# Optimization experiments

Hardware: AMD Instinct MI355X
Metric: run time of the kernel (lower is better)

## Reference

```python
import jax, jax.numpy as jnp
import numpy as np

BANK = 64
SHAPE = (512, 2048)
BATCH = 64
SELECTED = 4


def setup_inputs() -> dict:
    key = jax.random.key(0)
    k1, k2, k3 = jax.random.split(key, 3)
    parameter = jax.random.normal(k1, (*SHAPE, BANK), dtype=jnp.float32)
    selection_index = jax.random.randint(k2, (BATCH, SELECTED), 0, BANK)
    selection_probabilities = jax.random.uniform(k3, (BATCH, SELECTED), dtype=jnp.float32)
    return {
        "parameter": parameter,
        "selection_index": selection_index,
        "selection_probabilities": selection_probabilities,
    }


def reference(parameter, selection_index, selection_probabilities):
    # parameter: (*SHAPE, bank) -> move bank dim to front: (bank, *SHAPE)
    banked = jnp.moveaxis(parameter, -1, 0)
    # gather selected banks: (batch, selected, *SHAPE)
    gathered = banked[selection_index]
    # weighted sum over the selected dim (probabilities broadcast over data dims)
    out = jnp.einsum("bsij,bs->bij", gathered, selection_probabilities)
    return out
```

## Files before the change

kernel.cpp:

```cpp
#include <hip/hip_runtime.h>


#define NPOS   (512 * 2048)
#define NBANK  64
#define NBATCH 64
#define TILE   256
#define BLK    512

typedef float  f32x4 __attribute__((ext_vector_type(4)));
typedef int    i32x4 __attribute__((ext_vector_type(4)));

__global__ __launch_bounds__(BLK, 4) void vparam_kernel(
    const float* __restrict__ param,
    const int*   __restrict__ sel,
    const float* __restrict__ prob,
    float*       __restrict__ out)
{
    __shared__ float lds[NBANK * TILE];

    const int tid       = threadIdx.x;
    const int tile_base = blockIdx.x * TILE;

    const f32x4* g4 = (const f32x4*)(param + (size_t)tile_base * NBANK);
    #pragma unroll
    for (int i = 0; i < 8; ++i) {
        f32x4 v = __builtin_nontemporal_load(&g4[i * BLK + tid]);
        int p  = i * 32 + (tid >> 4);
        int k0 = (tid & 15) * 4;
        #pragma unroll
        for (int j = 0; j < 4; ++j) {
            int k = k0 + j;
            lds[k * TILE + (p ^ (k & 28))] = v[j];
        }
    }
    __syncthreads();

    const int wave = tid >> 6;
    const int lane = tid & 63;
    const int pw   = lane * 4;
    const i32x4* sel4  = (const i32x4*)sel;
    const f32x4* prob4 = (const f32x4*)prob;

    #pragma unroll
    for (int j = 0; j < 8; ++j) {
        int b = __builtin_amdgcn_readfirstlane(wave * 8 + j);
        i32x4 iv = sel4[b];
        f32x4 wv = prob4[b];
        const f32x4 a0 = *(const f32x4*)&lds[iv.x * TILE + (pw ^ (iv.x & 28))];
        const f32x4 a1 = *(const f32x4*)&lds[iv.y * TILE + (pw ^ (iv.y & 28))];
        const f32x4 a2 = *(const f32x4*)&lds[iv.z * TILE + (pw ^ (iv.z & 28))];
        const f32x4 a3 = *(const f32x4*)&lds[iv.w * TILE + (pw ^ (iv.w & 28))];
        f32x4 acc = a0 * wv.x + a1 * wv.y + a2 * wv.z + a3 * wv.w;
        f32x4* o = (f32x4*)(out + (size_t)b * NPOS + tile_base);
        __builtin_nontemporal_store(acc, &o[lane]);
    }
}

extern "C" void kernel_launch(void* const* d_in, const int* in_sizes, int n_in,
                              void* d_out, int out_size, void* d_ws, size_t ws_size,
                              hipStream_t stream) {
    const float* param = (const float*)d_in[0];
    const int*   sel   = (const int*)d_in[1];
    const float* prob  = (const float*)d_in[2];
    float*       out   = (float*)d_out;

    dim3 grid(NPOS / TILE);
    vparam_kernel<<<grid, BLK, 0, stream>>>(param, sel, prob, out);
}
```

Baseline: 96.25 us.

## Persistent blocks with register-prefetched next tile overlapping compute and stores

Switches from one block per tile to a fixed grid of 512 persistent blocks, each processing 8 tiles in sequence. The next tile's parameter data is loaded into registers while the current tile is computed from LDS and written out, then committed to LDS after a barrier. This is meant to hide global load latency behind the output stores. It costs extra registers, and occupancy is lowered from 4 to 2 blocks per CU in the launch bounds.

```diff
diff --git a/kernel.cpp b/kernel.cpp
--- a/kernel.cpp
+++ b/kernel.cpp
@@ -6,11 +6,13 @@
 #define NBATCH 64
 #define TILE   256
 #define BLK    512
+#define NBLK   512
+#define TPB    (NPOS / TILE / NBLK)
 
-typedef float  f32x4 __attribute__((ext_vector_type(4)));
-typedef int    i32x4 __attribute__((ext_vector_type(4)));
+typedef float f32x4 __attribute__((ext_vector_type(4)));
+typedef int   i32x4 __attribute__((ext_vector_type(4)));
 
-__global__ __launch_bounds__(BLK, 4) void vparam_kernel(
+__global__ __launch_bounds__(BLK, 2) void vparam_kernel(
     const float* __restrict__ param,
     const int*   __restrict__ sel,
     const float* __restrict__ prob,
@@ -18,41 +20,74 @@
 {
     __shared__ float lds[NBANK * TILE];
 
-    const int tid       = threadIdx.x;
-    const int tile_base = blockIdx.x * TILE;
-
-    const f32x4* g4 = (const f32x4*)(param + (size_t)tile_base * NBANK);
-    #pragma unroll
-    for (int i = 0; i < 8; ++i) {
-        f32x4 v = __builtin_nontemporal_load(&g4[i * BLK + tid]);
-        int p  = i * 32 + (tid >> 4);
-        int k0 = (tid & 15) * 4;
-        #pragma unroll
-        for (int j = 0; j < 4; ++j) {
-            int k = k0 + j;
-            lds[k * TILE + (p ^ (k & 28))] = v[j];
-        }
-    }
-    __syncthreads();
-
+    const int tid  = threadIdx.x;
     const int wave = tid >> 6;
     const int lane = tid & 63;
     const int pw   = lane * 4;
+    const int sp   = tid >> 4;
+    const int k0   = (tid & 15) * 4;
+
     const i32x4* sel4  = (const i32x4*)sel;
     const f32x4* prob4 = (const f32x4*)prob;
 
-    #pragma unroll
-    for (int j = 0; j < 8; ++j) {
-        int b = __builtin_amdgcn_readfirstlane(wave * 8 + j);
-        i32x4 iv = sel4[b];
-        f32x4 wv = prob4[b];
-        const f32x4 a0 = *(const f32x4*)&lds[iv.x * TILE + (pw ^ (iv.x & 28))];
-        const f32x4 a1 = *(const f32x4*)&lds[iv.y * TILE + (pw ^ (iv.y & 28))];
-        const f32x4 a2 = *(const f32x4*)&lds[iv.z * TILE + (pw ^ (iv.z & 28))];
-        const f32x4 a3 = *(const f32x4*)&lds[iv.w * TILE + (pw ^ (iv.w & 28))];
-        f32x4 acc = a0 * wv.x + a1 * wv.y + a2 * wv.z + a3 * wv.w;
-        f32x4* o = (f32x4*)(out + (size_t)b * NPOS + tile_base);
-        __builtin_nontemporal_store(acc, &o[lane]);
+    f32x4 r[8];
+    int tile = blockIdx.x * TPB;
+
+    {
+        const f32x4* g4 = (const f32x4*)(param + (size_t)tile * (TILE * NBANK));
+        #pragma unroll
+        for (int i = 0; i < 8; ++i)
+            r[i] = __builtin_nontemporal_load(&g4[i * BLK + tid]);
+        #pragma unroll
+        for (int i = 0; i < 8; ++i) {
+            int p = i * 32 + sp;
+            #pragma unroll
+            for (int j = 0; j < 4; ++j) {
+                int k = k0 + j;
+                lds[k * TILE + (p ^ (k & 28))] = r[i][j];
+            }
+        }
+    }
+
+    #pragma unroll 1
+    for (int t = 0; t < TPB; ++t) {
+        __syncthreads();
+
+        if (t + 1 < TPB) {
+            const f32x4* g4 = (const f32x4*)(param + (size_t)(tile + 1) * (TILE * NBANK));
+            #pragma unroll
+            for (int i = 0; i < 8; ++i)
+                r[i] = __builtin_nontemporal_load(&g4[i * BLK + tid]);
+        }
+
+        const size_t obase = (size_t)tile * TILE;
+        #pragma unroll
+        for (int j = 0; j < 8; ++j) {
+            int b = __builtin_amdgcn_readfirstlane(wave * 8 + j);
+            i32x4 iv = sel4[b];
+            f32x4 wv = prob4[b];
+            f32x4 a0 = *(const f32x4*)&lds[iv.x * TILE + (pw ^ (iv.x & 28))];
+            f32x4 a1 = *(const f32x4*)&lds[iv.y * TILE + (pw ^ (iv.y & 28))];
+            f32x4 a2 = *(const f32x4*)&lds[iv.z * TILE + (pw ^ (iv.z & 28))];
+            f32x4 a3 = *(const f32x4*)&lds[iv.w * TILE + (pw ^ (iv.w & 28))];
+            f32x4 acc = a0 * wv.x + a1 * wv.y + a2 * wv.z + a3 * wv.w;
+            __builtin_nontemporal_store(acc,
+                (f32x4*)(out + (size_t)b * NPOS + obase) + lane);
+        }
+
+        if (t + 1 < TPB) {
+            __syncthreads();
+            #pragma unroll
+            for (int i = 0; i < 8; ++i) {
+                int p = i * 32 + sp;
+                #pragma unroll
+                for (int j = 0; j < 4; ++j) {
+                    int k = k0 + j;
+                    lds[k * TILE + (p ^ (k & 28))] = r[i][j];
+                }
+            }
+        }
+        ++tile;
     }
 }
 
@@ -64,6 +99,5 @@
     const float* prob  = (const float*)d_in[2];
     float*       out   = (float*)d_out;
 
-    dim3 grid(NPOS / TILE);
-    vparam_kernel<<<grid, BLK, 0, stream>>>(param, sel, prob, out);
+    vparam_kernel<<<dim3(NBLK), dim3(BLK), 0, stream>>>(param, sel, prob, out);
 }
```

After: 131.2 us. 1.36x slower.
